# Performance work log

Hardware: AMD Instinct MI355X
Metric: run time of the kernel (lower is better)

The kernel has to match this reference:

```python
import jax, jax.numpy as jnp
import numpy as np

B, N, F_IN, F_OUT = 4, 4096, 300, 300


def setup_inputs() -> dict:
    key = jax.random.key(0)
    k1, k2, k3, k4 = jax.random.split(key, 4)
    text = jax.random.normal(k1, (B, N, F_IN), dtype=jnp.float32)
    adj = jax.random.uniform(k2, (B, N, N), dtype=jnp.float32)
    # parameters (the torch module leaves them uninitialized; use small random)
    weight = jax.random.normal(k3, (F_IN, F_OUT), dtype=jnp.float32) * (1.0 / np.sqrt(F_IN))
    bias = jax.random.normal(k4, (F_OUT,), dtype=jnp.float32) * 0.01
    return {"text": text, "adj": adj, "weight": weight, "bias": bias}


def reference(text, adj, weight, bias):
    # denom = rowsum(adj) + 1; D = diag(denom^-0.5) per batch
    # D @ adj @ D  ==  adj * d_i * d_j  (broadcast scaling, no dense diagonals)
    denom = jnp.sum(adj, axis=2) + 1.0            # [B, N]
    d = denom ** -0.5                              # [B, N]
    norm_adj = adj * d[:, :, None] * d[:, None, :]  # [B, N, N]
    # (norm_adj @ text) @ weight, contracted efficiently
    agg = jnp.matmul(norm_adj, text)               # [B, N, F_in]
    out = jnp.matmul(agg, weight) + bias           # [B, N, F_out]
    return out
```

## Files before the change

### kernel.cpp

```cpp
#include <hip/hip_runtime.h>
#include <hip/hip_bf16.h>

typedef __bf16 bf16x8 __attribute__((ext_vector_type(8)));
typedef __bf16 bf16x4 __attribute__((ext_vector_type(4)));
typedef float  f32x4  __attribute__((ext_vector_type(4)));

#define B_   4
#define N_   4096
#define FIN  300
#define FOUT 300
#define FP   320
#define MT   64
#define KT   64
#define NMT  (N_/MT)
#define NKT  (N_/KT)
#define TILE_BYTES (MT*KT*2)
#define YTILE 2048
#define STEP_B2 26624

#define WT_OFF   0
#define D_OFF    (512*1024)
#define TSC_OFF  (1024*1024)
#define YT_OFF   (16*1024*1024)
#define ADJB_OFF (32*1024*1024)
#define ADJB_BYTES ((size_t)B_ * N_ * N_ * 2)

#define SB() __builtin_amdgcn_sched_barrier(0)

__device__ __forceinline__ void gload_lds16(const void* g, void* l) {
    __builtin_amdgcn_global_load_lds((const __attribute__((address_space(1))) void*)g,
                                     (__attribute__((address_space(3))) void*)l, 16, 0, 0);
}

__global__ void k_wt(const float* __restrict__ W, __bf16* __restrict__ Wt) {
    int t = blockIdx.x * 256 + threadIdx.x;
    if (t >= FP * FP) return;
    int f = t / FP, k = t - f * FP;
    float v = (f < FOUT && k < FIN) ? W[k * FOUT + f] : 0.0f;
    Wt[t] = (__bf16)v;
}

__global__ void k_rowsum(const float* __restrict__ adj, float* __restrict__ d) {
    int row  = blockIdx.x * 4 + (threadIdx.x >> 6);
    int lane = threadIdx.x & 63;
    const float4* p = (const float4*)(adj + (size_t)row * N_);
    float s = 0.0f;
#pragma unroll
    for (int it = 0; it < 16; ++it) {
        float4 v = p[it * 64 + lane];
        s += v.x + v.y + v.z + v.w;
    }
#pragma unroll
    for (int off = 32; off; off >>= 1) s += __shfl_xor(s, off);
    if (lane == 0) d[row] = rsqrtf(s + 1.0f);
}

__global__ __launch_bounds__(512) void k_rowsum_cvt(const float* __restrict__ adj,
                                                    float* __restrict__ d,
                                                    char* __restrict__ adjb) {
    __shared__ __align__(16) char lds[4 * TILE_BYTES];
    const int mt = blockIdx.x, b = blockIdx.y;
    const int t = threadIdx.x, w = t >> 6, lane = t & 63;
    const int tloc = lane >> 4;
    const int chunk = (lane & 15) >> 1;
    const int sub8  = (lane & 1) * 8;
    const size_t rowbase = (size_t)b * N_ + mt * 64;
    char* gbase = adjb + (size_t)((b * NMT + mt) * NKT) * TILE_BYTES;

    float psum[8] = {};
    for (int g = 0; g < 16; ++g) {
#pragma unroll
        for (int rr = 0; rr < 8; ++rr) {
            int r = w * 8 + rr;
            float4 v = *(const float4*)(adj + (rowbase + r) * N_ + g * 256 + lane * 4);
            psum[rr] += v.x + v.y + v.z + v.w;
            bf16x4 o;
            o[0] = (__bf16)v.x; o[1] = (__bf16)v.y; o[2] = (__bf16)v.z; o[3] = (__bf16)v.w;
            int byte = tloc * TILE_BYTES + r * 128 + ((chunk * 16) ^ ((r & 7) << 4)) + sub8;
            *(bf16x4*)(lds + byte) = o;
        }
        __syncthreads();
#pragma unroll
        for (int i = 0; i < 4; ++i) {
            int idx = i * 512 + t;
            int tl = idx >> 9, off = (idx & 511) * 16;
            *(f32x4*)(gbase + (size_t)(g * 4 + tl) * TILE_BYTES + off) =
                *(const f32x4*)(lds + tl * TILE_BYTES + off);
        }
        __syncthreads();
    }
#pragma unroll
    for (int rr = 0; rr < 8; ++rr) {
        float s = psum[rr];
#pragma unroll
        for (int off = 32; off; off >>= 1) s += __shfl_xor(s, off);
        if (lane == 0) d[rowbase + w * 8 + rr] = rsqrtf(s + 1.0f);
    }
}

__global__ void k_tsc(const float* __restrict__ text, const float* __restrict__ d,
                      __bf16* __restrict__ Tsc) {
    int t = blockIdx.x * 256 + threadIdx.x;
    int j = t / FP;
    int k = t - j * FP;
    float v = 0.0f;
    if (k < FIN) v = d[j] * text[(size_t)j * FIN + k];
    Tsc[t] = (__bf16)v;
}

__global__ __launch_bounds__(256) void k_y(const __bf16* __restrict__ Wt,
                                           const __bf16* __restrict__ Tsc,
                                           __bf16* __restrict__ Yt) {
    int b    = blockIdx.y;
    int j0   = blockIdx.x * 64;
    int wave = threadIdx.x >> 6, lane = threadIdx.x & 63;
    int lr = lane & 15, lg = lane >> 4;
    f32x4 acc[5][4] = {};
    for (int k0 = 0; k0 < FP; k0 += 32) {
        bf16x8 a[5], bb[4];
#pragma unroll
        for (int fi = 0; fi < 5; ++fi) {
            int f = (wave * 5 + fi) * 16 + lr;
            a[fi] = *(const bf16x8*)(Wt + (size_t)f * FP + k0 + lg * 8);
        }
#pragma unroll
        for (int ji = 0; ji < 4; ++ji) {
            int j = j0 + ji * 16 + lr;
            bb[ji] = *(const bf16x8*)(Tsc + ((size_t)(b * N_ + j)) * FP + k0 + lg * 8);
        }
#pragma unroll
        for (int fi = 0; fi < 5; ++fi)
#pragma unroll
            for (int ji = 0; ji < 4; ++ji)
                acc[fi][ji] = __builtin_amdgcn_mfma_f32_16x16x32_bf16(a[fi], bb[ji], acc[fi][ji], 0, 0, 0);
    }
#pragma unroll
    for (int fi = 0; fi < 5; ++fi)
#pragma unroll
        for (int ji = 0; ji < 4; ++ji)
#pragma unroll
            for (int r = 0; r < 4; ++r) {
                int f = (wave * 5 + fi) * 16 + lg * 4 + r;
                int j = j0 + ji * 16 + lr;
                Yt[((size_t)b * FP + f) * N_ + j] = (__bf16)acc[fi][ji][r];
            }
}

__global__ __launch_bounds__(256) void k_y_t(const __bf16* __restrict__ Wt,
                                             const __bf16* __restrict__ Tsc,
                                             char* __restrict__ Ytt) {
    int b    = blockIdx.y;
    int j0   = blockIdx.x * 64;
    int wave = threadIdx.x >> 6, lane = threadIdx.x & 63;
    int lr = lane & 15, lg = lane >> 4;
    f32x4 acc[5][4] = {};
    for (int k0 = 0; k0 < FP; k0 += 32) {
        bf16x8 a[5], bb[4];
#pragma unroll
        for (int fi = 0; fi < 5; ++fi) {
            int f = (wave * 5 + fi) * 16 + lr;
            a[fi] = *(const bf16x8*)(Wt + (size_t)f * FP + k0 + lg * 8);
        }
#pragma unroll
        for (int ji = 0; ji < 4; ++ji) {
            int j = j0 + ji * 16 + lr;
            bb[ji] = *(const bf16x8*)(Tsc + ((size_t)(b * N_ + j)) * FP + k0 + lg * 8);
        }
#pragma unroll
        for (int fi = 0; fi < 5; ++fi)
#pragma unroll
            for (int ji = 0; ji < 4; ++ji)
                acc[fi][ji] = __builtin_amdgcn_mfma_f32_16x16x32_bf16(a[fi], bb[ji], acc[fi][ji], 0, 0, 0);
    }
#pragma unroll
    for (int fi = 0; fi < 5; ++fi)
#pragma unroll
        for (int ji = 0; ji < 4; ++ji)
#pragma unroll
            for (int r = 0; r < 4; ++r) {
                int f = (wave * 5 + fi) * 16 + lg * 4 + r;
                int j = j0 + ji * 16 + lr;
                int ft = f >> 4, floc = f & 15;
                int kt = j >> 6, jloc = j & 63;
                size_t base = (size_t)((b * 20 + ft) * 64 + kt) * YTILE;
                int byte = floc * 128 + (((jloc >> 3) * 16) ^ ((floc & 7) << 4)) + (jloc & 7) * 2;
                *(__bf16*)(Ytt + base + byte) = (__bf16)acc[fi][ji][r];
            }
}

__global__ __launch_bounds__(256) void k_gemm_pipe(const char* __restrict__ adjb,
                                                   const char* __restrict__ ytt,
                                                   const float* __restrict__ d,
                                                   const float* __restrict__ bias,
                                                   float* __restrict__ out) {
    __shared__ __align__(16) char smem[3 * STEP_B2];
    const int bid = blockIdx.x;
    const int bx  = bid & 31;
    const int b   = (bid >> 5) & 3;
    const int by  = bid >> 7;
    const int w = threadIdx.x >> 6, lane = threadIdx.x & 63;
    const int lr = lane & 15, lg = lane >> 4;

    const char* gp[7];
    int st[7], lo[7];
#pragma unroll
    for (int g = 0; g < 7; ++g) {
        int cid = w * 7 + g; if (cid >= 26) cid -= 26;
        if (cid < 16) {
            gp[g] = adjb + (size_t)((b * NMT + bx * 2 + (cid >> 3)) * NKT) * TILE_BYTES
                    + (cid & 7) * 1024 + lane * 16;
            st[g] = TILE_BYTES;
            lo[g] = cid * 1024;
        } else {
            int cc = cid - 16;
            gp[g] = ytt + (size_t)((b * 20 + by * 5 + (cc >> 1)) * 64) * YTILE
                    + (cc & 1) * 1024 + lane * 16;
            st[g] = YTILE;
            lo[g] = 16384 + cc * 1024;
        }
    }

    uint32_t sb = (uint32_t)(uintptr_t)(__attribute__((address_space(3))) char*)smem;
    const int sw = (lr & 7) << 4;
    const uint32_t col0 = (uint32_t)((lg * 16) ^ sw);
    const uint32_t col1 = (uint32_t)(((4 + lg) * 16) ^ sw);
    uint32_t rowA[2];
#pragma unroll
    for (int mi = 0; mi < 2; ++mi)
        rowA[mi] = sb + (w * 32 + mi * 16 + lr) * 128;
    uint32_t rowB[5];
#pragma unroll
    for (int nt = 0; nt < 5; ++nt) rowB[nt] = sb + 16384 + nt * YTILE + lr * 128;

    f32x4 acc[2][5] = {};
    uint32_t oc = 0, on = STEP_B2, ot = 2 * STEP_B2;

#pragma unroll
    for (int g = 0; g < 7; ++g) gload_lds16(gp[g], smem + lo[g]);
#pragma unroll
    for (int g = 0; g < 7; ++g) gload_lds16(gp[g] + st[g], smem + STEP_B2 + lo[g]);

    for (int t = 0; t < NKT; ++t) {
        int ks = t + 2 > NKT - 1 ? NKT - 1 : t + 2;
        SB();
#pragma unroll
        for (int g = 0; g < 7; ++g)
            gload_lds16(gp[g] + (size_t)ks * st[g], smem + ot + lo[g]);
        SB();
        asm volatile("s_waitcnt vmcnt(14)");
        SB();
        __builtin_amdgcn_s_barrier();
        bf16x8 af[2][2], bf[5][2];
#pragma unroll
        for (int mi = 0; mi < 2; ++mi) {
            asm volatile("ds_read_b128 %0, %1" : "=v"(af[mi][0]) : "v"(oc + rowA[mi] + col0));
            asm volatile("ds_read_b128 %0, %1" : "=v"(af[mi][1]) : "v"(oc + rowA[mi] + col1));
        }
#pragma unroll
        for (int nt = 0; nt < 5; ++nt) {
            asm volatile("ds_read_b128 %0, %1" : "=v"(bf[nt][0]) : "v"(oc + rowB[nt] + col0));
            asm volatile("ds_read_b128 %0, %1" : "=v"(bf[nt][1]) : "v"(oc + rowB[nt] + col1));
        }
        asm volatile("s_waitcnt lgkmcnt(0)");
        SB();
        __builtin_amdgcn_s_barrier();
        __builtin_amdgcn_s_setprio(1);
#pragma unroll
        for (int kh = 0; kh < 2; ++kh)
#pragma unroll
            for (int mi = 0; mi < 2; ++mi)
#pragma unroll
                for (int nt = 0; nt < 5; ++nt)
                    acc[mi][nt] = __builtin_amdgcn_mfma_f32_16x16x32_bf16(af[mi][kh], bf[nt][kh], acc[mi][nt], 0, 0, 0);
        __builtin_amdgcn_s_setprio(0);
        SB();
        uint32_t tmp = oc; oc = on; on = ot; ot = tmp;
    }

    const int rowb = bx * 128 + w * 32;
#pragma unroll
    for (int mi = 0; mi < 2; ++mi) {
        float di[4];
#pragma unroll
        for (int r = 0; r < 4; ++r)
            di[r] = d[b * N_ + rowb + mi * 16 + lg * 4 + r];
#pragma unroll
        for (int nt = 0; nt < 5; ++nt) {
            int f = by * 80 + nt * 16 + lr;
            if (f < FOUT) {
                float bv = bias[f];
#pragma unroll
                for (int r = 0; r < 4; ++r) {
                    int i = rowb + mi * 16 + lg * 4 + r;
                    out[((size_t)b * N_ + i) * FOUT + f] = di[r] * acc[mi][nt][r] + bv;
                }
            }
        }
    }
}

#define FB_LOAD(AV, BV, K0)                                                           \
    {                                                                                 \
        _Pragma("unroll")                                                             \
        for (int mi = 0; mi < 2; ++mi) {                                              \
            const float4* p = (const float4*)(adjf + (size_t)(rowbase + mi * 16 + lr) * N_ + (K0) + lg * 8); \
            float4 v0 = p[0], v1 = p[1];                                              \
            AV[mi][0] = (__bf16)v0.x; AV[mi][1] = (__bf16)v0.y;                       \
            AV[mi][2] = (__bf16)v0.z; AV[mi][3] = (__bf16)v0.w;                       \
            AV[mi][4] = (__bf16)v1.x; AV[mi][5] = (__bf16)v1.y;                       \
            AV[mi][6] = (__bf16)v1.z; AV[mi][7] = (__bf16)v1.w;                       \
        }                                                                             \
        _Pragma("unroll")                                                             \
        for (int nt = 0; nt < 10; ++nt) {                                             \
            int f = wn * 160 + nt * 16 + lr;                                          \
            BV[nt] = *(const bf16x8*)(Yb + (size_t)f * N_ + (K0) + lg * 8);           \
        }                                                                             \
    }
#define FB_MFMA(AV, BV)                                                               \
    {                                                                                 \
        _Pragma("unroll")                                                             \
        for (int mi = 0; mi < 2; ++mi)                                                \
            _Pragma("unroll")                                                         \
            for (int nt = 0; nt < 10; ++nt)                                           \
                acc[mi][nt] = __builtin_amdgcn_mfma_f32_16x16x32_bf16(AV[mi], BV[nt], acc[mi][nt], 0, 0, 0); \
    }

__global__ __launch_bounds__(256) void k_gemm_fb(const float* __restrict__ adj,
                                                 const __bf16* __restrict__ Yt,
                                                 const float* __restrict__ d,
                                                 const float* __restrict__ bias,
                                                 float* __restrict__ out) {
    int b    = blockIdx.y;
    int wave = threadIdx.x >> 6, lane = threadIdx.x & 63;
    int wm = wave & 1, wn = wave >> 1;
    int lr = lane & 15, lg = lane >> 4;
    int rowbase = blockIdx.x * 64 + wm * 32;
    const float*  adjf = adj + (size_t)b * N_ * N_;
    const __bf16* Yb   = Yt + (size_t)b * FP * N_;

    f32x4 acc[2][10] = {};
    bf16x8 aA[2], bA[10], aB[2], bB[10];

    FB_LOAD(aA, bA, 0)
    for (int k0 = 0; k0 < N_ - 64; k0 += 64) {
        FB_LOAD(aB, bB, k0 + 32)
        FB_MFMA(aA, bA)
        FB_LOAD(aA, bA, k0 + 64)
        FB_MFMA(aB, bB)
    }
    FB_LOAD(aB, bB, N_ - 32)
    FB_MFMA(aA, bA)
    FB_MFMA(aB, bB)

#pragma unroll
    for (int mi = 0; mi < 2; ++mi) {
        float di[4];
#pragma unroll
        for (int r = 0; r < 4; ++r)
            di[r] = d[b * N_ + rowbase + mi * 16 + lg * 4 + r];
#pragma unroll
        for (int nt = 0; nt < 10; ++nt) {
            int f = wn * 160 + nt * 16 + lr;
            if (f < FOUT) {
                float bv = bias[f];
#pragma unroll
                for (int r = 0; r < 4; ++r) {
                    int i = rowbase + mi * 16 + lg * 4 + r;
                    out[((size_t)b * N_ + i) * FOUT + f] = di[r] * acc[mi][nt][r] + bv;
                }
            }
        }
    }
}

extern "C" void kernel_launch(void* const* d_in, const int* in_sizes, int n_in,
                              void* d_out, int out_size, void* d_ws, size_t ws_size,
                              hipStream_t stream) {
    const float* text = (const float*)d_in[0];
    const float* adj  = (const float*)d_in[1];
    const float* W    = (const float*)d_in[2];
    const float* bias = (const float*)d_in[3];
    float* out = (float*)d_out;

    char* ws = (char*)d_ws;
    __bf16* Wt   = (__bf16*)(ws + WT_OFF);
    float*  dv   = (float*)(ws + D_OFF);
    __bf16* Tsc  = (__bf16*)(ws + TSC_OFF);
    char*   Ybuf = ws + YT_OFF;
    char*   adjb = ws + ADJB_OFF;

    bool big = ws_size >= (size_t)ADJB_OFF + ADJB_BYTES;

    k_wt<<<dim3((FP * FP + 255) / 256), dim3(256), 0, stream>>>(W, Wt);
    if (big)
        k_rowsum_cvt<<<dim3(NMT, B_), dim3(512), 0, stream>>>(adj, dv, adjb);
    else
        k_rowsum<<<dim3(B_ * N_ / 4), dim3(256), 0, stream>>>(adj, dv);
    k_tsc<<<dim3(B_ * N_ * FP / 256), dim3(256), 0, stream>>>(text, dv, Tsc);
    if (big) {
        k_y_t<<<dim3(N_ / 64, B_), dim3(256), 0, stream>>>(Wt, Tsc, Ybuf);
        k_gemm_pipe<<<dim3(512), dim3(256), 0, stream>>>(adjb, Ybuf, dv, bias, out);
    } else {
        k_y<<<dim3(N_ / 64, B_), dim3(256), 0, stream>>>(Wt, Tsc, (__bf16*)Ybuf);
        k_gemm_fb<<<dim3(N_ / 64, B_), dim3(256), 0, stream>>>(adj, (__bf16*)Ybuf, dv, bias, out);
    }
}
```

Measured before the change: 187.8 us.

## Load Y operand directly into registers instead of staging through LDS

```diff
diff --git a/kernel.cpp b/kernel.cpp
--- a/kernel.cpp
+++ b/kernel.cpp
@@ -15,8 +15,7 @@
 #define NMT  (N_/MT)
 #define NKT  (N_/KT)
 #define TILE_BYTES (MT*KT*2)
-#define YTILE 2048
-#define STEP_B2 26624
+#define STEP_A 16384
 
 #define WT_OFF   0
 #define D_OFF    (512*1024)
@@ -146,54 +145,12 @@
             }
 }
 
-__global__ __launch_bounds__(256) void k_y_t(const __bf16* __restrict__ Wt,
-                                             const __bf16* __restrict__ Tsc,
-                                             char* __restrict__ Ytt) {
-    int b    = blockIdx.y;
-    int j0   = blockIdx.x * 64;
-    int wave = threadIdx.x >> 6, lane = threadIdx.x & 63;
-    int lr = lane & 15, lg = lane >> 4;
-    f32x4 acc[5][4] = {};
-    for (int k0 = 0; k0 < FP; k0 += 32) {
-        bf16x8 a[5], bb[4];
-#pragma unroll
-        for (int fi = 0; fi < 5; ++fi) {
-            int f = (wave * 5 + fi) * 16 + lr;
-            a[fi] = *(const bf16x8*)(Wt + (size_t)f * FP + k0 + lg * 8);
-        }
-#pragma unroll
-        for (int ji = 0; ji < 4; ++ji) {
-            int j = j0 + ji * 16 + lr;
-            bb[ji] = *(const bf16x8*)(Tsc + ((size_t)(b * N_ + j)) * FP + k0 + lg * 8);
-        }
-#pragma unroll
-        for (int fi = 0; fi < 5; ++fi)
-#pragma unroll
-            for (int ji = 0; ji < 4; ++ji)
-                acc[fi][ji] = __builtin_amdgcn_mfma_f32_16x16x32_bf16(a[fi], bb[ji], acc[fi][ji], 0, 0, 0);
-    }
-#pragma unroll
-    for (int fi = 0; fi < 5; ++fi)
-#pragma unroll
-        for (int ji = 0; ji < 4; ++ji)
-#pragma unroll
-            for (int r = 0; r < 4; ++r) {
-                int f = (wave * 5 + fi) * 16 + lg * 4 + r;
-                int j = j0 + ji * 16 + lr;
-                int ft = f >> 4, floc = f & 15;
-                int kt = j >> 6, jloc = j & 63;
-                size_t base = (size_t)((b * 20 + ft) * 64 + kt) * YTILE;
-                int byte = floc * 128 + (((jloc >> 3) * 16) ^ ((floc & 7) << 4)) + (jloc & 7) * 2;
-                *(__bf16*)(Ytt + base + byte) = (__bf16)acc[fi][ji][r];
-            }
-}
-
 __global__ __launch_bounds__(256) void k_gemm_pipe(const char* __restrict__ adjb,
-                                                   const char* __restrict__ ytt,
+                                                   const __bf16* __restrict__ yt,
                                                    const float* __restrict__ d,
                                                    const float* __restrict__ bias,
                                                    float* __restrict__ out) {
-    __shared__ __align__(16) char smem[3 * STEP_B2];
+    __shared__ __align__(16) char smem[3 * STEP_A];
     const int bid = blockIdx.x;
     const int bx  = bid & 31;
     const int b   = (bid >> 5) & 3;
@@ -201,24 +158,20 @@
     const int w = threadIdx.x >> 6, lane = threadIdx.x & 63;
     const int lr = lane & 15, lg = lane >> 4;
 
-    const char* gp[7];
-    int st[7], lo[7];
-#pragma unroll
-    for (int g = 0; g < 7; ++g) {
-        int cid = w * 7 + g; if (cid >= 26) cid -= 26;
-        if (cid < 16) {
-            gp[g] = adjb + (size_t)((b * NMT + bx * 2 + (cid >> 3)) * NKT) * TILE_BYTES
-                    + (cid & 7) * 1024 + lane * 16;
-            st[g] = TILE_BYTES;
-            lo[g] = cid * 1024;
-        } else {
-            int cc = cid - 16;
-            gp[g] = ytt + (size_t)((b * 20 + by * 5 + (cc >> 1)) * 64) * YTILE
-                    + (cc & 1) * 1024 + lane * 16;
-            st[g] = YTILE;
-            lo[g] = 16384 + cc * 1024;
-        }
-    }
+    const char* gpA[4];
+    int loA[4];
+#pragma unroll
+    for (int g = 0; g < 4; ++g) {
+        int cid = w * 4 + g;
+        gpA[g] = adjb + (size_t)((b * NMT + bx * 2 + (cid >> 3)) * NKT) * TILE_BYTES
+                 + (cid & 7) * 1024 + lane * 16;
+        loA[g] = cid * 1024;
+    }
+
+    const __bf16* bp[5];
+#pragma unroll
+    for (int nt = 0; nt < 5; ++nt)
+        bp[nt] = yt + ((size_t)b * FP + by * 80 + nt * 16 + lr) * N_ + lg * 8;
 
     uint32_t sb = (uint32_t)(uintptr_t)(__attribute__((address_space(3))) char*)smem;
     const int sw = (lr & 7) << 4;
@@ -228,53 +181,58 @@
 #pragma unroll
     for (int mi = 0; mi < 2; ++mi)
         rowA[mi] = sb + (w * 32 + mi * 16 + lr) * 128;
-    uint32_t rowB[5];
-#pragma unroll
-    for (int nt = 0; nt < 5; ++nt) rowB[nt] = sb + 16384 + nt * YTILE + lr * 128;
 
     f32x4 acc[2][5] = {};
-    uint32_t oc = 0, on = STEP_B2, ot = 2 * STEP_B2;
-
-#pragma unroll
-    for (int g = 0; g < 7; ++g) gload_lds16(gp[g], smem + lo[g]);
-#pragma unroll
-    for (int g = 0; g < 7; ++g) gload_lds16(gp[g] + st[g], smem + STEP_B2 + lo[g]);
-
-    for (int t = 0; t < NKT; ++t) {
-        int ks = t + 2 > NKT - 1 ? NKT - 1 : t + 2;
-        SB();
-#pragma unroll
-        for (int g = 0; g < 7; ++g)
-            gload_lds16(gp[g] + (size_t)ks * st[g], smem + ot + lo[g]);
-        SB();
-        asm volatile("s_waitcnt vmcnt(14)");
-        SB();
-        __builtin_amdgcn_s_barrier();
-        bf16x8 af[2][2], bf[5][2];
-#pragma unroll
-        for (int mi = 0; mi < 2; ++mi) {
-            asm volatile("ds_read_b128 %0, %1" : "=v"(af[mi][0]) : "v"(oc + rowA[mi] + col0));
-            asm volatile("ds_read_b128 %0, %1" : "=v"(af[mi][1]) : "v"(oc + rowA[mi] + col1));
-        }
-#pragma unroll
-        for (int nt = 0; nt < 5; ++nt) {
-            asm volatile("ds_read_b128 %0, %1" : "=v"(bf[nt][0]) : "v"(oc + rowB[nt] + col0));
-            asm volatile("ds_read_b128 %0, %1" : "=v"(bf[nt][1]) : "v"(oc + rowB[nt] + col1));
-        }
-        asm volatile("s_waitcnt lgkmcnt(0)");
-        SB();
-        __builtin_amdgcn_s_barrier();
-        __builtin_amdgcn_s_setprio(1);
-#pragma unroll
-        for (int kh = 0; kh < 2; ++kh)
-#pragma unroll
-            for (int mi = 0; mi < 2; ++mi)
-#pragma unroll
-                for (int nt = 0; nt < 5; ++nt)
-                    acc[mi][nt] = __builtin_amdgcn_mfma_f32_16x16x32_bf16(af[mi][kh], bf[nt][kh], acc[mi][nt], 0, 0, 0);
-        __builtin_amdgcn_s_setprio(0);
-        SB();
-        uint32_t tmp = oc; oc = on; on = ot; ot = tmp;
+    bf16x8 B0[5][2], B1[5][2];
+    uint32_t oc = 0, on = STEP_A, ot = 2 * STEP_A;
+
+#define STAGEA(OFF, KT_) { _Pragma("unroll") \
+    for (int g = 0; g < 4; ++g) \
+        gload_lds16(gpA[g] + (size_t)(KT_) * TILE_BYTES, smem + (OFF) + loA[g]); }
+
+#define LOADB(BS, kt) { _Pragma("unroll") \
+    for (int nt = 0; nt < 5; ++nt) { \
+        BS[nt][0] = *(const bf16x8*)(bp[nt] + (size_t)(kt) * 64); \
+        BS[nt][1] = *(const bf16x8*)(bp[nt] + (size_t)(kt) * 64 + 32); } }
+
+#define PHASE(BSc, BSn, T)                                                              \
+    {                                                                                   \
+        int ks = (T) + 2 > NKT - 1 ? NKT - 1 : (T) + 2;                                 \
+        int kb = (T) + 1 > NKT - 1 ? NKT - 1 : (T) + 1;                                 \
+        SB();                                                                           \
+        STAGEA(ot, ks)                                                                  \
+        LOADB(BSn, kb)                                                                  \
+        SB();                                                                           \
+        asm volatile("s_waitcnt vmcnt(14)");   \
+        SB();                                                                           \
+        __builtin_amdgcn_s_barrier();               \
+        bf16x8 af[2][2];                                                                \
+        asm volatile("ds_read_b128 %0, %1" : "=v"(af[0][0]) : "v"(oc + rowA[0] + col0));\
+        asm volatile("ds_read_b128 %0, %1" : "=v"(af[0][1]) : "v"(oc + rowA[0] + col1));\
+        asm volatile("ds_read_b128 %0, %1" : "=v"(af[1][0]) : "v"(oc + rowA[1] + col0));\
+        asm volatile("ds_read_b128 %0, %1" : "=v"(af[1][1]) : "v"(oc + rowA[1] + col1));\
+        asm volatile("s_waitcnt lgkmcnt(0)");                                           \
+        SB();                                   \
+        __builtin_amdgcn_s_barrier();                  \
+        __builtin_amdgcn_s_setprio(1);                                                  \
+        _Pragma("unroll")                                                               \
+        for (int kh = 0; kh < 2; ++kh)                                                  \
+            _Pragma("unroll")                                                           \
+            for (int mi = 0; mi < 2; ++mi)                                              \
+                _Pragma("unroll")                                                       \
+                for (int nt = 0; nt < 5; ++nt)                                          \
+                    acc[mi][nt] = __builtin_amdgcn_mfma_f32_16x16x32_bf16(af[mi][kh], BSc[nt][kh], acc[mi][nt], 0, 0, 0); \
+        __builtin_amdgcn_s_setprio(0);                                                  \
+        SB();                                                                           \
+        uint32_t tmp_ = oc; oc = on; on = ot; ot = tmp_;                                \
+    }
+
+    STAGEA(0, 0)
+    STAGEA(STEP_A, 1)
+    LOADB(B0, 0)
+    for (int t = 0; t < NKT; t += 2) {
+        PHASE(B0, B1, t)
+        PHASE(B1, B0, t + 1)
     }
 
     const int rowb = bx * 128 + w * 32;
@@ -297,6 +255,9 @@
             }
         }
     }
+#undef STAGEA
+#undef LOADB
+#undef PHASE
 }
 
 #define FB_LOAD(AV, BV, K0)                                                           \
@@ -386,7 +347,7 @@
     __bf16* Wt   = (__bf16*)(ws + WT_OFF);
     float*  dv   = (float*)(ws + D_OFF);
     __bf16* Tsc  = (__bf16*)(ws + TSC_OFF);
-    char*   Ybuf = ws + YT_OFF;
+    __bf16* Yt   = (__bf16*)(ws + YT_OFF);
     char*   adjb = ws + ADJB_OFF;
 
     bool big = ws_size >= (size_t)ADJB_OFF + ADJB_BYTES;
@@ -397,11 +358,9 @@
     else
         k_rowsum<<<dim3(B_ * N_ / 4), dim3(256), 0, stream>>>(adj, dv);
     k_tsc<<<dim3(B_ * N_ * FP / 256), dim3(256), 0, stream>>>(text, dv, Tsc);
-    if (big) {
-        k_y_t<<<dim3(N_ / 64, B_), dim3(256), 0, stream>>>(Wt, Tsc, Ybuf);
-        k_gemm_pipe<<<dim3(512), dim3(256), 0, stream>>>(adjb, Ybuf, dv, bias, out);
-    } else {
-        k_y<<<dim3(N_ / 64, B_), dim3(256), 0, stream>>>(Wt, Tsc, (__bf16*)Ybuf);
-        k_gemm_fb<<<dim3(N_ / 64, B_), dim3(256), 0, stream>>>(adj, (__bf16*)Ybuf, dv, bias, out);
-    }
-}
+    k_y<<<dim3(N_ / 64, B_), dim3(256), 0, stream>>>(Wt, Tsc, Yt);
+    if (big)
+        k_gemm_pipe<<<dim3(512), dim3(256), 0, stream>>>(adjb, Yt, dv, bias, out);
+    else
+        k_gemm_fb<<<dim3(N_ / 64, B_), dim3(256), 0, stream>>>(adj, Yt, dv, bias, out);
+}
```

After: 285.1 us. 1.52x slower.
